# Optimization experiments

Hardware: AMD Instinct MI355X
Metric: run time of the kernel (lower is better)

The kernel has to match this reference:

```python
import jax, jax.numpy as jnp
import numpy as np

BN_EPS = 1e-5

def setup_inputs() -> dict:
    key = jax.random.key(0)
    ks = jax.random.split(key, 16)
    B, N = 64, 1024
    dims = [3, 64, 128, 256]
    H = 256
    inp = {"x": jax.random.normal(ks[0], (B, dims[0], N), dtype=jnp.float32)}
    for i in range(3):
        ci, co = dims[i], dims[i + 1]
        inp[f"w{i+1}"] = jax.random.normal(ks[1 + i], (co, ci), dtype=jnp.float32) * (1.0 / np.sqrt(ci))
        inp[f"b{i+1}"] = jnp.zeros((co,), dtype=jnp.float32)
        inp[f"g{i+1}"] = jnp.ones((co,), dtype=jnp.float32)
        inp[f"be{i+1}"] = jnp.zeros((co,), dtype=jnp.float32)
    inp["A"] = jnp.eye(H, dtype=jnp.float32) + 0.01 * jax.random.normal(ks[10], (H, H), dtype=jnp.float32)
    inp["Bm"] = 0.01 * jax.random.normal(ks[11], (H, dims[-1]), dtype=jnp.float32)
    inp["Cm"] = 0.01 * jax.random.normal(ks[12], (dims[-1], H), dtype=jnp.float32)
    return inp


def _conv_bn_relu(h, w, b, g, be):
    # h: [B, Cin, N]; 1x1 conv == channel matmul
    y = jnp.einsum('oi,bin->bon', w, h) + b[None, :, None]
    mu = jnp.mean(y, axis=(0, 2), keepdims=True)
    var = jnp.var(y, axis=(0, 2), keepdims=True)
    y = (y - mu) * jax.lax.rsqrt(var + BN_EPS)
    y = y * g[None, :, None] + be[None, :, None]
    return jax.nn.relu(y)


def reference(x, w1, b1, g1, be1, w2, b2, g2, be2, w3, b3, g3, be3, A, Bm, Cm):
    h = _conv_bn_relu(x, w1, b1, g1, be1)
    h = _conv_bn_relu(h, w2, b2, g2, be2)
    h = _conv_bn_relu(h, w3, b3, g3, be3)
    u = jnp.transpose(h, (0, 2, 1))  # [B, N, C]
    Bsz = u.shape[0]
    H = A.shape[0]
    A_norm = A / (jnp.linalg.norm(A, ord=2) + 1e-5)
    uB = u @ Bm.T  # precompute input projection: [B, N, H]

    def step(hstate, ut):
        hstate = jax.nn.relu(hstate @ A_norm.T + ut)
        return hstate, hstate @ Cm.T

    h0 = jnp.zeros((Bsz, H), dtype=x.dtype)
    _, ys = jax.lax.scan(step, h0, jnp.transpose(uB, (1, 0, 2)))  # ys: [N, B, Cout]
    y = jnp.transpose(ys, (1, 2, 0))  # [B, Cout, N]
    return y
```

## Files before the change

### kernel.cpp

```cpp
#include <hip/hip_runtime.h>

#define B_SZ 64
#define N_SZ 1024
#define C1   64
#define C2   128
#define C3   256
#define H_SZ 256

__global__ void k_btb(const float* __restrict__ A, float* __restrict__ B0) {
  int i = blockIdx.x;
  int j = threadIdx.x;
  float acc = 0.f;
  for (int k = 0; k < 256; ++k)
    acc = fmaf(A[k * 256 + i], A[k * 256 + j], acc);
  B0[i * 256 + j] = acc;
}

__global__ void k_bsq(const float* __restrict__ Bin, float* __restrict__ Bout) {
  __shared__ float diag[256];
  int i = blockIdx.x, j = threadIdx.x;
  diag[j] = Bin[j * 256 + j];
  __syncthreads();
  float tr = 0.f;
  for (int k = 0; k < 256; ++k) tr += diag[k];
  float inv = 1.0f / tr;
  float acc = 0.f;
  for (int k = 0; k < 256; ++k)
    acc = fmaf(Bin[i * 256 + k], Bin[k * 256 + j], acc);
  Bout[i * 256 + j] = acc * inv * inv;
}

__global__ void k_sfin(const float* __restrict__ Bf, const float* __restrict__ B0,
                       float* __restrict__ sinv) {
  __shared__ float v[256], w[256];
  __shared__ float red[256];
  __shared__ int redi[256];
  int t = threadIdx.x;
  red[t] = Bf[t * 256 + t];
  redi[t] = t;
  __syncthreads();
  for (int s = 128; s > 0; s >>= 1) {
    if (t < s) {
      if (red[t + s] > red[t]) { red[t] = red[t + s]; redi[t] = redi[t + s]; }
    }
    __syncthreads();
  }
  int jmax = redi[0];
  __syncthreads();
  v[t] = Bf[t * 256 + jmax];
  __syncthreads();
  float acc = 0.f;
  for (int k = 0; k < 256; ++k) acc = fmaf(B0[t * 256 + k], v[k], acc);
  w[t] = acc;
  __syncthreads();
  red[t] = v[t] * w[t];
  __syncthreads();
  for (int s = 128; s > 0; s >>= 1) { if (t < s) red[t] += red[t + s]; __syncthreads(); }
  float num = red[0];
  __syncthreads();
  red[t] = v[t] * v[t];
  __syncthreads();
  for (int s = 128; s > 0; s >>= 1) { if (t < s) red[t] += red[t + s]; __syncthreads(); }
  if (t == 0) {
    float lam = num / red[0];
    float sg = sqrtf(lam);
    *sinv = 1.0f / (sg + 1e-5f);
  }
}

__global__ void k_conv1(const float* __restrict__ x, const float* __restrict__ w,
                        const float* __restrict__ bias, float* __restrict__ y) {
  int b = blockIdx.x >> 2;
  int n = ((blockIdx.x & 3) << 8) + threadIdx.x;
  const float* xb = x + (size_t)b * 3 * N_SZ;
  float x0 = xb[n], x1 = xb[N_SZ + n], x2 = xb[2 * N_SZ + n];
  float* yb = y + (size_t)b * C1 * N_SZ;
#pragma unroll 4
  for (int o = 0; o < C1; ++o) {
    float r = fmaf(w[o * 3 + 0], x0,
              fmaf(w[o * 3 + 1], x1,
              fmaf(w[o * 3 + 2], x2, bias[o])));
    yb[(size_t)o * N_SZ + n] = r;
  }
}

__global__ void k_stats(const float* __restrict__ y, int C,
                        const float* __restrict__ g, const float* __restrict__ be,
                        float* __restrict__ coef) {
  int c = blockIdx.x;
  int t = threadIdx.x;
  float s1 = 0.f, s2 = 0.f;
  for (int b = 0; b < B_SZ; ++b) {
    const float4* p = (const float4*)(y + ((size_t)b * C + c) * N_SZ);
    float4 v = p[t];
    s1 += v.x + v.y + v.z + v.w;
    s2 += v.x * v.x + v.y * v.y + v.z * v.z + v.w * v.w;
  }
  __shared__ float r1[256], r2[256];
  r1[t] = s1; r2[t] = s2;
  __syncthreads();
  for (int s = 128; s > 0; s >>= 1) {
    if (t < s) { r1[t] += r1[t + s]; r2[t] += r2[t + s]; }
    __syncthreads();
  }
  if (t == 0) {
    const float M = (float)(B_SZ * N_SZ);
    float mu = r1[0] / M;
    float var = r2[0] / M - mu * mu;
    float sc = g[c] * rsqrtf(var + 1e-5f);
    coef[c] = sc;
    coef[C + c] = be[c] - mu * sc;
  }
}


#define GEMM_COMPUTE8(ATc, BTc)                                      \
  _Pragma("unroll") for (int kk = 0; kk < 8; ++kk) {                 \
    float av[2][4], bv[2][4];                                        \
    *(float4*)av[0] = *(const float4*)&ATc[kk][ty * 4];              \
    *(float4*)av[1] = *(const float4*)&ATc[kk][64 + ty * 4];         \
    *(float4*)bv[0] = *(const float4*)&BTc[kk][tx * 4];              \
    *(float4*)bv[1] = *(const float4*)&BTc[kk][64 + tx * 4];         \
    _Pragma("unroll") for (int p = 0; p < 2; ++p)                    \
      _Pragma("unroll") for (int q = 0; q < 2; ++q)                  \
        _Pragma("unroll") for (int i = 0; i < 4; ++i)                \
          _Pragma("unroll") for (int j = 0; j < 4; ++j)              \
            acc[p][q][i][j] = fmaf(av[p][i], bv[q][j], acc[p][q][i][j]); \
  }

#define RAW_BARRIER()                                    \
  asm volatile("s_waitcnt lgkmcnt(0)" ::: "memory");     \
  __builtin_amdgcn_s_barrier();                          \
  asm volatile("" ::: "memory");

template <int K, int CO>
__global__ __launch_bounds__(256, 3) void k_convG(
    const float* __restrict__ hin, const float* __restrict__ coef,
    const float* __restrict__ w, const float* __restrict__ bias,
    float* __restrict__ y) {
  __shared__ float At[2][8][132];
  __shared__ float Bt[2][8][132];
  const int n0 = blockIdx.x * 128, o0 = blockIdx.y * 128, b = blockIdx.z;
  const int t = threadIdx.x, tx = t & 15, ty = t >> 4;
  const int wo = t & 127, wk = (t >> 7) * 4;
  const int hr = t >> 5, hc = (t & 31) * 4;
  const float* hb = hin + (size_t)b * K * N_SZ + n0;
  float acc[2][2][4][4] = {};
  float4 wreg = *(const float4*)(w + (size_t)(o0 + wo) * K + wk);
  float4 hreg = *(const float4*)(hb + (size_t)hr * N_SZ + hc);
  float scR = coef[hr], shR = coef[K + hr];
  At[0][wk + 0][wo] = wreg.x; At[0][wk + 1][wo] = wreg.y;
  At[0][wk + 2][wo] = wreg.z; At[0][wk + 3][wo] = wreg.w;
  {
    float4 u;
    u.x = fmaxf(fmaf(hreg.x, scR, shR), 0.f);
    u.y = fmaxf(fmaf(hreg.y, scR, shR), 0.f);
    u.z = fmaxf(fmaf(hreg.z, scR, shR), 0.f);
    u.w = fmaxf(fmaf(hreg.w, scR, shR), 0.f);
    *(float4*)&Bt[0][hr][hc] = u;
  }
  __syncthreads();
  constexpr int NT = K / 8;
  for (int kt = 0; kt < NT; ++kt) {
    const int cur = kt & 1;
    if (kt + 1 < NT) {
      const int k0 = (kt + 1) * 8;
      wreg = *(const float4*)(w + (size_t)(o0 + wo) * K + k0 + wk);
      hreg = *(const float4*)(hb + (size_t)(k0 + hr) * N_SZ + hc);
      scR = coef[k0 + hr]; shR = coef[K + k0 + hr];
    }
    GEMM_COMPUTE8(At[cur], Bt[cur]);
    if (kt + 1 < NT) {
      const int nx = cur ^ 1;
      At[nx][wk + 0][wo] = wreg.x; At[nx][wk + 1][wo] = wreg.y;
      At[nx][wk + 2][wo] = wreg.z; At[nx][wk + 3][wo] = wreg.w;
      float4 u;
      u.x = fmaxf(fmaf(hreg.x, scR, shR), 0.f);
      u.y = fmaxf(fmaf(hreg.y, scR, shR), 0.f);
      u.z = fmaxf(fmaf(hreg.z, scR, shR), 0.f);
      u.w = fmaxf(fmaf(hreg.w, scR, shR), 0.f);
      *(float4*)&Bt[nx][hr][hc] = u;
      RAW_BARRIER();
    }
  }
#pragma unroll
  for (int p = 0; p < 2; ++p)
#pragma unroll
    for (int i = 0; i < 4; ++i) {
      const int row = o0 + p * 64 + ty * 4 + i;
      const float bvv = bias[row];
      float* yr = y + ((size_t)b * CO + row) * N_SZ + n0;
      float4 v0 = {acc[p][0][i][0] + bvv, acc[p][0][i][1] + bvv,
                   acc[p][0][i][2] + bvv, acc[p][0][i][3] + bvv};
      float4 v1 = {acc[p][1][i][0] + bvv, acc[p][1][i][1] + bvv,
                   acc[p][1][i][2] + bvv, acc[p][1][i][3] + bvv};
      *(float4*)(yr + tx * 4) = v0;
      *(float4*)(yr + 64 + tx * 4) = v1;
    }
}

__global__ __launch_bounds__(256, 3) void k_uBG(
    const float* __restrict__ y3, const float* __restrict__ coef,
    const float* __restrict__ Bm, float* __restrict__ uB) {
  __shared__ float Xt[2][8][132];
  __shared__ float Bt[2][8][132];
  const int n0 = blockIdx.x * 128, h0 = blockIdx.y * 128, b = blockIdx.z;
  const int t = threadIdx.x, tx = t & 15, ty = t >> 4;
  const int xr = t >> 5, xc = (t & 31) * 4;
  const int bh = t & 127, bk = (t >> 7) * 4;
  const float* yb = y3 + (size_t)b * C3 * N_SZ + n0;
  float acc[2][2][4][4] = {};
  float4 xreg = *(const float4*)(yb + (size_t)xr * N_SZ + xc);
  float scR = coef[xr], shR = coef[C3 + xr];
  float4 breg = *(const float4*)(Bm + (size_t)(h0 + bh) * C3 + bk);
  {
    float4 u;
    u.x = fmaxf(fmaf(xreg.x, scR, shR), 0.f);
    u.y = fmaxf(fmaf(xreg.y, scR, shR), 0.f);
    u.z = fmaxf(fmaf(xreg.z, scR, shR), 0.f);
    u.w = fmaxf(fmaf(xreg.w, scR, shR), 0.f);
    *(float4*)&Xt[0][xr][xc] = u;
    Bt[0][bk + 0][bh] = breg.x; Bt[0][bk + 1][bh] = breg.y;
    Bt[0][bk + 2][bh] = breg.z; Bt[0][bk + 3][bh] = breg.w;
  }
  __syncthreads();
  constexpr int NT = C3 / 8;
  for (int kt = 0; kt < NT; ++kt) {
    const int cur = kt & 1;
    if (kt + 1 < NT) {
      const int c0 = (kt + 1) * 8;
      xreg = *(const float4*)(yb + (size_t)(c0 + xr) * N_SZ + xc);
      scR = coef[c0 + xr]; shR = coef[C3 + c0 + xr];
      breg = *(const float4*)(Bm + (size_t)(h0 + bh) * C3 + c0 + bk);
    }
    GEMM_COMPUTE8(Xt[cur], Bt[cur]);
    if (kt + 1 < NT) {
      const int nx = cur ^ 1;
      float4 u;
      u.x = fmaxf(fmaf(xreg.x, scR, shR), 0.f);
      u.y = fmaxf(fmaf(xreg.y, scR, shR), 0.f);
      u.z = fmaxf(fmaf(xreg.z, scR, shR), 0.f);
      u.w = fmaxf(fmaf(xreg.w, scR, shR), 0.f);
      *(float4*)&Xt[nx][xr][xc] = u;
      Bt[nx][bk + 0][bh] = breg.x; Bt[nx][bk + 1][bh] = breg.y;
      Bt[nx][bk + 2][bh] = breg.z; Bt[nx][bk + 3][bh] = breg.w;
      RAW_BARRIER();
    }
  }
#pragma unroll
  for (int p = 0; p < 2; ++p)
#pragma unroll
    for (int i = 0; i < 4; ++i) {
      const int nrow = n0 + p * 64 + ty * 4 + i;
      float* orow = uB + ((size_t)b * N_SZ + nrow) * H_SZ + h0;
      *(float4*)(orow + tx * 4) = *(float4*)acc[p][0][i];
      *(float4*)(orow + 64 + tx * 4) = *(float4*)acc[p][1][i];
    }
}

__global__ __launch_bounds__(256, 3) void k_ymmG(
    const float* __restrict__ hs, const float* __restrict__ Cm,
    float* __restrict__ y) {
  __shared__ float Ct[2][8][132];
  __shared__ float Ht[2][8][132];
  const int n0 = blockIdx.x * 128, co0 = blockIdx.y * 128, b = blockIdx.z;
  const int t = threadIdx.x, tx = t & 15, ty = t >> 4;
  const int cc = t & 127, ck = (t >> 7) * 4;
  const float* hbase = hs + ((size_t)b * N_SZ + n0) * H_SZ;
  float acc[2][2][4][4] = {};
  float4 creg = *(const float4*)(Cm + (size_t)(co0 + cc) * H_SZ + ck);
  float4 hreg = *(const float4*)(hbase + (size_t)cc * H_SZ + ck);
  Ct[0][ck + 0][cc] = creg.x; Ct[0][ck + 1][cc] = creg.y;
  Ct[0][ck + 2][cc] = creg.z; Ct[0][ck + 3][cc] = creg.w;
  Ht[0][ck + 0][cc] = hreg.x; Ht[0][ck + 1][cc] = hreg.y;
  Ht[0][ck + 2][cc] = hreg.z; Ht[0][ck + 3][cc] = hreg.w;
  __syncthreads();
  constexpr int NT = H_SZ / 8;
  for (int kt = 0; kt < NT; ++kt) {
    const int cur = kt & 1;
    if (kt + 1 < NT) {
      const int h0 = (kt + 1) * 8;
      creg = *(const float4*)(Cm + (size_t)(co0 + cc) * H_SZ + h0 + ck);
      hreg = *(const float4*)(hbase + (size_t)cc * H_SZ + h0 + ck);
    }
    GEMM_COMPUTE8(Ct[cur], Ht[cur]);
    if (kt + 1 < NT) {
      const int nx = cur ^ 1;
      Ct[nx][ck + 0][cc] = creg.x; Ct[nx][ck + 1][cc] = creg.y;
      Ct[nx][ck + 2][cc] = creg.z; Ct[nx][ck + 3][cc] = creg.w;
      Ht[nx][ck + 0][cc] = hreg.x; Ht[nx][ck + 1][cc] = hreg.y;
      Ht[nx][ck + 2][cc] = hreg.z; Ht[nx][ck + 3][cc] = hreg.w;
      RAW_BARRIER();
    }
  }
#pragma unroll
  for (int p = 0; p < 2; ++p)
#pragma unroll
    for (int i = 0; i < 4; ++i) {
      const int row = co0 + p * 64 + ty * 4 + i;
      float* yr = y + ((size_t)b * C3 + row) * N_SZ + n0;
      *(float4*)(yr + tx * 4) = *(float4*)acc[p][0][i];
      *(float4*)(yr + 64 + tx * 4) = *(float4*)acc[p][1][i];
    }
}

__global__ __launch_bounds__(512, 1) void k_scan(
    const float* __restrict__ A, const float* __restrict__ sinvp,
    const float* __restrict__ uB, float* __restrict__ hs) {
  __shared__ float h_lds[256];
  __shared__ float part[8][256];
  const int b = blockIdx.x;
  const int t = threadIdx.x;
  const int lane = t & 63;
  const int wv = t >> 6;
  const float sinv = *sinvp;
  float areg[4][32];
#pragma unroll
  for (int k = 0; k < 4; ++k) {
    const float* r = A + (size_t)(lane + 64 * k) * 256 + wv * 32;
#pragma unroll
    for (int j = 0; j < 32; ++j) areg[k][j] = r[j] * sinv;
  }
  if (t < 256) h_lds[t] = 0.f;
  __syncthreads();
  const float* ub = uB + (size_t)b * N_SZ * H_SZ;
  float* ho = hs + (size_t)b * N_SZ * H_SZ;
  float u_cur = (t < 256) ? ub[t] : 0.f;
  for (int s = 0; s < N_SZ; ++s) {
    float u_next = 0.f;
    if (t < 256 && s + 1 < N_SZ) u_next = ub[(size_t)(s + 1) * H_SZ + t];
    const float4* hp = ((const float4*)h_lds) + wv * 8;
    float acc[4] = {0.f, 0.f, 0.f, 0.f};
#pragma unroll
    for (int q = 0; q < 8; ++q) {
      const float4 h4 = hp[q];
#pragma unroll
      for (int k = 0; k < 4; ++k) {
        acc[k] = fmaf(areg[k][q * 4 + 0], h4.x, acc[k]);
        acc[k] = fmaf(areg[k][q * 4 + 1], h4.y, acc[k]);
        acc[k] = fmaf(areg[k][q * 4 + 2], h4.z, acc[k]);
        acc[k] = fmaf(areg[k][q * 4 + 3], h4.w, acc[k]);
      }
    }
    part[wv][lane] = acc[0];
    part[wv][lane + 64] = acc[1];
    part[wv][lane + 128] = acc[2];
    part[wv][lane + 192] = acc[3];
    asm volatile("s_waitcnt lgkmcnt(0)" ::: "memory");
    __builtin_amdgcn_s_barrier();
    if (t < 256) {
      float p = u_cur;
#pragma unroll
      for (int c = 0; c < 8; ++c) p += part[c][t];
      p = fmaxf(p, 0.f);
      h_lds[t] = p;
      ho[(size_t)s * H_SZ + t] = p;
    }
    u_cur = u_next;
    asm volatile("s_waitcnt lgkmcnt(0)" ::: "memory");
    __builtin_amdgcn_s_barrier();
  }
}

extern "C" void kernel_launch(void* const* d_in, const int* in_sizes, int n_in,
                              void* d_out, int out_size, void* d_ws, size_t ws_size,
                              hipStream_t stream) {
  const float* x   = (const float*)d_in[0];
  const float* w1  = (const float*)d_in[1];
  const float* b1  = (const float*)d_in[2];
  const float* g1  = (const float*)d_in[3];
  const float* be1 = (const float*)d_in[4];
  const float* w2  = (const float*)d_in[5];
  const float* b2  = (const float*)d_in[6];
  const float* g2  = (const float*)d_in[7];
  const float* be2 = (const float*)d_in[8];
  const float* w3  = (const float*)d_in[9];
  const float* b3  = (const float*)d_in[10];
  const float* g3  = (const float*)d_in[11];
  const float* be3 = (const float*)d_in[12];
  const float* A   = (const float*)d_in[13];
  const float* Bm  = (const float*)d_in[14];
  const float* Cm  = (const float*)d_in[15];
  float* out = (float*)d_out;

  char* ws = (char*)d_ws;
  const size_t MB = 1024ull * 1024ull;
  float* y1 = (float*)(ws + 0);
  float* y2 = (float*)(ws + 16 * MB);
  float* y3 = (float*)(ws + 48 * MB);
  float* hs = (float*)(ws + 0);
  char* sp = ws + 112 * MB;
  float* B0 = (float*)(sp);
  float* P  = (float*)(sp + 256 * 1024);
  float* Q  = (float*)(sp + 512 * 1024);
  float* sinv  = (float*)(sp + 768 * 1024);
  float* coef1 = (float*)(sp + 768 * 1024 + 1024);
  float* coef2 = (float*)(sp + 768 * 1024 + 4096);
  float* coef3 = (float*)(sp + 768 * 1024 + 8192);

  k_btb<<<256, 256, 0, stream>>>(A, B0);
  {
    float* bufs[2] = {P, Q};
    const float* cur = B0;
    for (int it = 0; it < 12; ++it) {
      float* nxt = bufs[it & 1];
      k_bsq<<<256, 256, 0, stream>>>(cur, nxt);
      cur = nxt;
    }
    k_sfin<<<1, 256, 0, stream>>>(cur, B0, sinv);
  }

  k_conv1<<<dim3(B_SZ * 4), 256, 0, stream>>>(x, w1, b1, y1);
  k_stats<<<C1, 256, 0, stream>>>(y1, C1, g1, be1, coef1);
  k_convG<C1, C2><<<dim3(8, 1, B_SZ), 256, 0, stream>>>(y1, coef1, w2, b2, y2);
  k_stats<<<C2, 256, 0, stream>>>(y2, C2, g2, be2, coef2);
  k_convG<C2, C3><<<dim3(8, 2, B_SZ), 256, 0, stream>>>(y2, coef2, w3, b3, y3);
  k_stats<<<C3, 256, 0, stream>>>(y3, C3, g3, be3, coef3);

  k_uBG<<<dim3(8, 2, B_SZ), 256, 0, stream>>>(y3, coef3, Bm, out);

  k_scan<<<dim3(B_SZ), 512, 0, stream>>>(A, sinv, out, hs);

  k_ymmG<<<dim3(8, 2, B_SZ), 256, 0, stream>>>(hs, Cm, out);
}
```

Before: 1.123 ms.

## Remove second barrier in scan via double-buffered partials and readlane broadcast

The recurrent scan kernel now has each wave redundantly reduce the 8 partial sums for its own 32 hidden indices. It then broadcasts the new state to all lanes with readlane, so the state lives in scalar registers and is no longer stored to and reloaded from LDS. Double-buffering the partial array lets it drop the second block barrier per step, which cuts per-step sync latency on this latency-bound serial loop. In exchange every wave repeats the reduction work and issues 32 readlanes per step, and the code relies on the double buffer to avoid a write-after-read race.

```diff
diff --git a/kernel.cpp b/kernel.cpp
--- a/kernel.cpp
+++ b/kernel.cpp
@@ -307,8 +307,7 @@
 __global__ __launch_bounds__(512, 1) void k_scan(
     const float* __restrict__ A, const float* __restrict__ sinvp,
     const float* __restrict__ uB, float* __restrict__ hs) {
-  __shared__ float h_lds[256];
-  __shared__ float part[8][256];
+  __shared__ float part[2][8][256];
   const int b = blockIdx.x;
   const int t = threadIdx.x;
   const int lane = t & 63;
@@ -321,44 +320,50 @@
 #pragma unroll
     for (int j = 0; j < 32; ++j) areg[k][j] = r[j] * sinv;
   }
-  if (t < 256) h_lds[t] = 0.f;
-  __syncthreads();
+  const int jl = lane & 31;
+  const int i_r = wv * 32 + jl;
   const float* ub = uB + (size_t)b * N_SZ * H_SZ;
   float* ho = hs + (size_t)b * N_SZ * H_SZ;
-  float u_cur = (t < 256) ? ub[t] : 0.f;
+  float u_cur = ub[i_r];
+  float hsv[32];
+#pragma unroll
+  for (int p = 0; p < 32; ++p) hsv[p] = 0.f;
+  __syncthreads();
   for (int s = 0; s < N_SZ; ++s) {
     float u_next = 0.f;
-    if (t < 256 && s + 1 < N_SZ) u_next = ub[(size_t)(s + 1) * H_SZ + t];
-    const float4* hp = ((const float4*)h_lds) + wv * 8;
-    float acc[4] = {0.f, 0.f, 0.f, 0.f};
-#pragma unroll
-    for (int q = 0; q < 8; ++q) {
-      const float4 h4 = hp[q];
-#pragma unroll
-      for (int k = 0; k < 4; ++k) {
-        acc[k] = fmaf(areg[k][q * 4 + 0], h4.x, acc[k]);
-        acc[k] = fmaf(areg[k][q * 4 + 1], h4.y, acc[k]);
-        acc[k] = fmaf(areg[k][q * 4 + 2], h4.z, acc[k]);
-        acc[k] = fmaf(areg[k][q * 4 + 3], h4.w, acc[k]);
-      }
-    }
-    part[wv][lane] = acc[0];
-    part[wv][lane + 64] = acc[1];
-    part[wv][lane + 128] = acc[2];
-    part[wv][lane + 192] = acc[3];
+    if (s + 1 < N_SZ) u_next = ub[(size_t)(s + 1) * H_SZ + i_r];
+    float acc0 = 0.f, acc1 = 0.f, acc2 = 0.f, acc3 = 0.f;
+#pragma unroll
+    for (int p = 0; p < 32; ++p) {
+      acc0 = fmaf(areg[0][p], hsv[p], acc0);
+      acc1 = fmaf(areg[1][p], hsv[p], acc1);
+      acc2 = fmaf(areg[2][p], hsv[p], acc2);
+      acc3 = fmaf(areg[3][p], hsv[p], acc3);
+    }
+    const int buf = s & 1;
+    part[buf][wv][lane] = acc0;
+    part[buf][wv][lane + 64] = acc1;
+    part[buf][wv][lane + 128] = acc2;
+    part[buf][wv][lane + 192] = acc3;
     asm volatile("s_waitcnt lgkmcnt(0)" ::: "memory");
     __builtin_amdgcn_s_barrier();
-    if (t < 256) {
-      float p = u_cur;
-#pragma unroll
-      for (int c = 0; c < 8; ++c) p += part[c][t];
-      p = fmaxf(p, 0.f);
-      h_lds[t] = p;
-      ho[(size_t)s * H_SZ + t] = p;
-    }
+    asm volatile("" ::: "memory");
+    float q0 = part[buf][0][i_r];
+    float q1 = part[buf][1][i_r];
+    float q2 = part[buf][2][i_r];
+    float q3 = part[buf][3][i_r];
+    float q4 = part[buf][4][i_r];
+    float q5 = part[buf][5][i_r];
+    float q6 = part[buf][6][i_r];
+    float q7 = part[buf][7][i_r];
+    float sum = ((q0 + q1) + (q2 + q3)) + ((q4 + q5) + (q6 + q7));
+    float pv = fmaxf(sum + u_cur, 0.f);
+    if (jl == lane) ho[(size_t)s * H_SZ + i_r] = pv;
+#pragma unroll
+    for (int p = 0; p < 32; ++p)
+      hsv[p] = __uint_as_float(
+          __builtin_amdgcn_readlane(__float_as_uint(pv), p));
     u_cur = u_next;
-    asm volatile("s_waitcnt lgkmcnt(0)" ::: "memory");
-    __builtin_amdgcn_s_barrier();
   }
 }
 
```

Result: slower. 1.294 ms (+15.1%).
